# Performance work log

Measured on AMD Instinct MI355X. Metric: run time of the kernel, lower is better.

Reference implementation:

```python
import jax, jax.numpy as jnp
import numpy as np

N_NODES = 50000
N_ENT = 100000
N_REL = 200
DE = 100
DR = 100
B = 16
E2 = 600000
U = 500


def setup_inputs() -> dict:
    key = jax.random.key(0)
    ks = jax.random.split(key, 16)
    f32 = jnp.float32
    return {
        "entity_table": jax.random.normal(ks[0], (N_ENT, DE), f32),
        "relation_table": jax.random.normal(ks[1], (N_REL, DR), f32),
        "total_unseen_embedding": jax.random.normal(ks[2], (U, DE), f32),
        "att_mu": jax.random.normal(ks[3], (2 * N_REL, B), f32) * 0.1,
        "basis_mu": jax.random.normal(ks[4], (B, DE + DR, DE), f32) * 0.05,
        "root_mu": jax.random.normal(ks[5], (DE, DE), f32) * 0.1,
        "bias_mu": jnp.zeros((DE,), f32),
        "att_sigma": jax.random.normal(ks[6], (2 * N_REL, B), f32) * 0.1,
        "basis_sigma": jax.random.normal(ks[7], (B, DE + DR, DE), f32) * 0.05,
        "root_sigma": jax.random.normal(ks[8], (DE, DE), f32) * 0.1,
        "bias_sigma": jnp.zeros((DE,), f32),
        "node_id": jax.random.randint(ks[9], (N_NODES,), 0, N_ENT),
        "edge_index": jax.random.randint(ks[10], (2, E2), 0, N_NODES),
        "edge_type": jax.random.randint(ks[11], (E2,), 0, 2 * N_REL),
        "rel_index": jax.random.randint(ks[12], (E2,), 0, N_REL),
        "unseen_index": jax.random.randint(ks[13], (U,), 0, N_NODES),
    }


def gen_conv(m, edge_type, dst, x, att, basis, root, bias, n_nodes):
    """Basis-decomposed relational conv with mean aggregation (GENConv).

    m: [E, in] per-edge concat(x_src, rel_emb); msg_e = m_e @ (att[type_e] @ basis).
    Computed as sum_b coeff[:, b] * (m @ basis[b]) to avoid an [E, in, out] gather.
    """
    coeff = att[edge_type]  # [E, B]
    msg = coeff[:, 0:1] * (m @ basis[0])
    for b in range(1, basis.shape[0]):
        msg = msg + coeff[:, b:b + 1] * (m @ basis[b])
    agg = jax.ops.segment_sum(msg, dst, num_segments=n_nodes)  # [N, out]
    cnt = jax.ops.segment_sum(jnp.ones((m.shape[0],), m.dtype), dst,
                              num_segments=n_nodes)
    agg = agg / jnp.maximum(cnt, 1.0)[:, None]  # scatter-mean, empty nodes -> 0
    return agg + x @ root + bias


def reference(entity_table, relation_table, total_unseen_embedding,
              att_mu, basis_mu, root_mu, bias_mu,
              att_sigma, basis_sigma, root_sigma, bias_sigma,
              node_id, edge_index, edge_type, rel_index, unseen_index):
    x = entity_table[node_id]  # [N, De]
    x = x.at[unseen_index].set(total_unseen_embedding)
    rel_emb = relation_table[rel_index]  # [E, Dr]
    src, dst = edge_index[0], edge_index[1]
    m = jnp.concatenate([x[src], rel_emb], axis=1)  # [E, De+Dr]
    n = x.shape[0]
    mu = gen_conv(m, edge_type, dst, x, att_mu, basis_mu, root_mu, bias_mu, n)
    logvar = gen_conv(m, edge_type, dst, x, att_sigma, basis_sigma,
                      root_sigma, bias_sigma, n)
    # eval mode: reparameterize -> mu, dropout -> identity
    unseen = mu[unseen_index]
    return unseen, mu[unseen_index], logvar[unseen_index]
```

## Files before the change

### kernel.cpp

```cpp
#include <hip/hip_runtime.h>
#include <stdint.h>

#define E2V     600000
#define NNODES  50000
#define UCNT    500
#define DE      100
#define DOUT    100
#define NB      16
#define KTOT    3328
#define KCH     104
#define MROWS   512
#define HASHN   2048
#define HCAP    64
#define NREG    586
#define ECAP    96
#define TRB     832

using short8 = __attribute__((ext_vector_type(8))) short;
using f32x4  = __attribute__((ext_vector_type(4))) float;

static constexpr size_t align256(size_t x){ return (x + 255) & ~size_t(255); }
static constexpr size_t OFF_HCNT = 0;
static constexpr size_t OFF_IHEA = align256(OFF_HCNT + NREG*4);
static constexpr size_t OFF_INEX = OFF_IHEA + MROWS*4;
static constexpr size_t OFF_HBUF = align256(OFF_INEX + MROWS*4);
static constexpr size_t OFF_GM   = align256(OFF_HBUF + (size_t)NREG*HCAP*4);
static constexpr size_t OFF_GS   = OFF_GM + (size_t)MROWS*KTOT*2;
static constexpr size_t OFF_BTM  = align256(OFF_GS + (size_t)MROWS*KTOT*2);
static constexpr size_t OFF_BTS  = OFF_BTM + (size_t)DOUT*KTOT*2;

__device__ __forceinline__ unsigned short f2b(float f){
    uint32_t u = __float_as_uint(f);
    uint32_t r = (u + 0x7FFFu + ((u >> 16) & 1u)) >> 16;
    return (unsigned short)r;
}

__device__ __forceinline__ uint32_t hh(int key){
    return (((uint32_t)key * 2654435761u) >> 16) & (HASHN - 1);
}
__device__ __forceinline__ void hins(int* hk, int* hv, int key, int val){
    uint32_t idx = hh(key);
    while (true){
        int k = hk[idx];
        if (k == key){ atomicMax(&hv[idx], val); return; }
        if (k == -1){
            int old = atomicCAS(&hk[idx], -1, key);
            if (old == -1 || old == key){ atomicMax(&hv[idx], val); return; }
        }
        idx = (idx + 1) & (HASHN - 1);
    }
}
__device__ __forceinline__ int hlook(const int* hk, const int* hv, int key){
    uint32_t idx = hh(key);
    while (true){
        int k = hk[idx];
        if (k == key) return hv[idx];
        if (k == -1)  return -1;
        idx = (idx + 1) & (HASHN - 1);
    }
}

__device__ __forceinline__ float bt_src(const float* __restrict__ basis,
                                        const float* __restrict__ root,
                                        const float* __restrict__ bias,
                                        int k, int j){
    if (j >= 100) return 0.f;
    if (k < 3200) return basis[k*100 + j];
    if (k < 3300) return root[(k-3200)*100 + j];
    if (k == 3300) return bias[j];
    return 0.f;
}

__global__ __launch_bounds__(256) void k1(
        const int* __restrict__ unseen_index, const int* __restrict__ eidx,
        int* __restrict__ hcnt, uint32_t* __restrict__ hbuf,
        int* __restrict__ ihead, int* __restrict__ inext,
        const float* __restrict__ bm, const float* __restrict__ bs,
        const float* __restrict__ rm, const float* __restrict__ rs,
        const float* __restrict__ qm, const float* __restrict__ qs,
        unsigned short* __restrict__ btm, unsigned short* __restrict__ bts){
    __shared__ int hk[HASHN], hv[HASHN];
    __shared__ float tile[32][33];
    __shared__ uint32_t sHit[HCAP];
    __shared__ int sN, sIH[MROWS];
    int bx = blockIdx.x, tid = threadIdx.x;

    if (bx < NREG){
        for (int i = tid; i < HASHN; i += 256){ hk[i] = -1; hv[i] = -1; }
        if (tid == 0) sN = 0;
        __syncthreads();
        for (int u = tid; u < UCNT; u += 256) hins(hk, hv, unseen_index[u], u);
        __syncthreads();
        int e0 = bx*1024 + tid*4;
        if (e0 < E2V){
            int4 d = *(const int4*)(eidx + E2V + e0);
            int s;
            s = hlook(hk, hv, d.x); if (s >= 0){ int p = atomicAdd(&sN,1); if (p < HCAP) sHit[p] = ((uint32_t)s<<21)|(uint32_t)(e0);   }
            s = hlook(hk, hv, d.y); if (s >= 0){ int p = atomicAdd(&sN,1); if (p < HCAP) sHit[p] = ((uint32_t)s<<21)|(uint32_t)(e0+1); }
            s = hlook(hk, hv, d.z); if (s >= 0){ int p = atomicAdd(&sN,1); if (p < HCAP) sHit[p] = ((uint32_t)s<<21)|(uint32_t)(e0+2); }
            s = hlook(hk, hv, d.w); if (s >= 0){ int p = atomicAdd(&sN,1); if (p < HCAP) sHit[p] = ((uint32_t)s<<21)|(uint32_t)(e0+3); }
        }
        __syncthreads();
        int n = sN < HCAP ? sN : HCAP;
        if (tid == 0) hcnt[bx] = n;
        if (tid < n) hbuf[bx*HCAP + tid] = sHit[tid];
        return;
    }
    if (bx < NREG + TRB){
        int b2 = bx - NREG;
        int kt = b2 % KCH, jt = (b2 / KCH) & 3, br = b2 / (KCH*4);
        const float* basis = br ? bs : bm;
        const float* root  = br ? rs : rm;
        const float* bias  = br ? qs : qm;
        unsigned short* bt = br ? bts : btm;
        int k0 = kt*32, j0 = jt*32;
        int tx = tid & 31, ty = tid >> 5;
        for (int r = ty; r < 32; r += 8)
            tile[r][tx] = bt_src(basis, root, bias, k0 + r, j0 + tx);
        __syncthreads();
        for (int r = ty; r < 32; r += 8){
            int j = j0 + r;
            if (j < 100) bt[(size_t)j*KTOT + k0 + tx] = f2b(tile[tx][r]);
        }
        return;
    }
    for (int i = tid; i < HASHN; i += 256){ hk[i] = -1; hv[i] = -1; }
    for (int i = tid; i < MROWS; i += 256) sIH[i] = -1;
    __syncthreads();
    for (int u = tid; u < UCNT; u += 256) hins(hk, hv, unseen_index[u], u);
    __syncthreads();
    for (int u = tid; u < UCNT; u += 256){
        int slot = hlook(hk, hv, unseen_index[u]);
        inext[u] = atomicExch(&sIH[slot], u);
    }
    __syncthreads();
    for (int i = tid; i < MROWS; i += 256) ihead[i] = sIH[i];
}

__global__ __launch_bounds__(256) void k_g(
        const int* __restrict__ hcnt, const uint32_t* __restrict__ hbuf,
        const int* __restrict__ unseen_index,
        const int* __restrict__ eidx,
        const int* __restrict__ etype, const int* __restrict__ rel_index,
        const int* __restrict__ node_id,
        const float* __restrict__ ent, const float* __restrict__ unseen,
        const float* __restrict__ rel,
        const float* __restrict__ am, const float* __restrict__ as_,
        unsigned short* __restrict__ Gm, unsigned short* __restrict__ Gs){
    int slot = blockIdx.x;
    int tid  = threadIdx.x;
    __shared__ int hk[HASHN], hv[HASHN];
    __shared__ int sEdge[ECAP], sNE;
    __shared__ __align__(16) float sM[8][200];
    __shared__ __align__(16) float sAm[8][16], sAs[8][16];
    __shared__ const float* sPX[8];
    __shared__ const float* sPR[8];
    __shared__ int sT[8];

    for (int i = tid; i < HASHN; i += 256){ hk[i] = -1; hv[i] = -1; }
    if (tid == 0) sNE = 0;
    __syncthreads();
    for (int u = tid; u < UCNT; u += 256) hins(hk, hv, unseen_index[u], u);
    __syncthreads();
    for (int r = tid; r < NREG; r += 256){
        int c = hcnt[r];
        for (int i = 0; i < c; ++i){
            uint32_t h = hbuf[r*HCAP + i];
            if ((int)(h >> 21) == slot){
                int p = atomicAdd(&sNE, 1);
                if (p < ECAP) sEdge[p] = (int)(h & 0x1FFFFFu);
            }
        }
    }
    __syncthreads();
    int nT = sNE;
    int nE = nT > ECAP ? ECAP : nT;

    float gm[16], gs[16];
    #pragma unroll
    for (int b = 0; b < NB; ++b){ gm[b] = 0.f; gs[b] = 0.f; }

    for (int c0 = 0; c0 < nE; c0 += 8){
        int kc = nE - c0; if (kc > 8) kc = 8;
        if (tid < kc){
            int e = sEdge[c0 + tid];
            sT[tid] = etype[e];
            int s = eidx[e];
            int p = hlook(hk, hv, s);
            sPX[tid] = (p >= 0) ? unseen + (size_t)p*DE : ent + (size_t)node_id[s]*DE;
            sPR[tid] = rel + (size_t)rel_index[e]*DE;
        }
        __syncthreads();
        for (int q = tid; q < kc*50; q += 256){
            int eL = q / 50, s = q % 50;
            const float* base = (s < 25) ? sPX[eL] : sPR[eL];
            int off = (s < 25) ? s*4 : (s-25)*4;
            float4 v = *(const float4*)(base + off);
            int kb = (s < 25) ? s*4 : (s-25)*4 + 100;
            *(float4*)&sM[eL][kb] = v;
        }
        if (tid < kc*16){
            int eL = tid >> 4, b = tid & 15;
            int t = sT[eL];
            sAm[eL][b] = am[t*NB + b];
            sAs[eL][b] = as_[t*NB + b];
        }
        __syncthreads();
        if (tid < 200){
            for (int e = 0; e < kc; ++e){
                float mk = sM[e][tid];
                const float4* pa = (const float4*)&sAm[e][0];
                const float4* ps = (const float4*)&sAs[e][0];
                #pragma unroll
                for (int q = 0; q < 4; ++q){
                    float4 va = pa[q], vs = ps[q];
                    gm[q*4+0] += va.x*mk; gm[q*4+1] += va.y*mk;
                    gm[q*4+2] += va.z*mk; gm[q*4+3] += va.w*mk;
                    gs[q*4+0] += vs.x*mk; gs[q*4+1] += vs.y*mk;
                    gs[q*4+2] += vs.z*mk; gs[q*4+3] += vs.w*mk;
                }
            }
        }
        __syncthreads();
    }
    size_t row = (size_t)slot * KTOT;
    float inv = 1.f / fmaxf((float)nT, 1.f);
    if (tid < 200){
        #pragma unroll
        for (int b = 0; b < NB; ++b){
            Gm[row + b*200 + tid] = f2b(gm[b] * inv);
            Gs[row + b*200 + tid] = f2b(gs[b] * inv);
        }
    }
    if (tid < 100){
        float xv = (slot < UCNT) ? unseen[(size_t)slot*DE + tid] : 0.f;
        unsigned short h = f2b(xv);
        Gm[row + 3200 + tid] = h; Gs[row + 3200 + tid] = h;
    } else if (tid == 100){
        Gm[row + 3300] = f2b(1.f); Gs[row + 3300] = f2b(1.f);
    } else if (tid > 100 && tid < 128){
        Gm[row + 3200 + tid] = 0; Gs[row + 3200 + tid] = 0;
    }
}

__global__ __launch_bounds__(512) void k_gemm(
        const unsigned short* __restrict__ Gm, const unsigned short* __restrict__ Gs,
        const unsigned short* __restrict__ Btm, const unsigned short* __restrict__ Bts,
        const int* __restrict__ ihead, const int* __restrict__ inext,
        float* __restrict__ out){
    __shared__ f32x4 red[512];
    int bid = blockIdx.x;
    int br  = bid / 224;
    int w2  = bid % 224;
    int m16 = w2 & 31;
    int jt  = w2 >> 5;
    int wv  = threadIdx.x >> 6;
    int lane = threadIdx.x & 63;
    const unsigned short* A  = br ? Gs : Gm;
    const unsigned short* Bt = br ? Bts : Btm;
    int rowa = lane & 15, ko = (lane >> 4) * 8;
    int j0 = (jt == 6) ? 84 : jt*16;
    int col = j0 + rowa;
    const unsigned short* ap = A  + (size_t)(m16*16 + rowa)*KTOT + ko + wv*416;
    const unsigned short* bp = Bt + (size_t)col*KTOT + ko + wv*416;
    f32x4 acc = {0.f, 0.f, 0.f, 0.f};
    #pragma unroll
    for (int kc = 0; kc < 13; ++kc){
        short8 av = *(const short8*)(ap + kc*32);
        short8 bv = *(const short8*)(bp + kc*32);
        acc = __builtin_amdgcn_mfma_f32_16x16x32_bf16(av, bv, acc, 0, 0, 0);
    }
    red[threadIdx.x] = acc;
    __syncthreads();
    if (threadIdx.x < 64){
        #pragma unroll
        for (int w = 1; w < 8; ++w){
            f32x4 o = red[threadIdx.x + w*64];
            acc[0] += o[0]; acc[1] += o[1]; acc[2] += o[2]; acc[3] += o[3];
        }
        if (jt < 6 || col >= 96){
            int r0 = m16*16 + (lane >> 4)*4;
            #pragma unroll
            for (int r = 0; r < 4; ++r){
                int u = ihead[r0 + r];
                while (u >= 0){
                    if (br == 0){
                        out[(size_t)u*100 + col] = acc[r];
                        out[(size_t)(UCNT + u)*100 + col] = acc[r];
                    } else {
                        out[(size_t)(2*UCNT + u)*100 + col] = acc[r];
                    }
                    u = inext[u];
                }
            }
        }
    }
}

extern "C" void kernel_launch(void* const* d_in, const int* in_sizes, int n_in,
                              void* d_out, int out_size, void* d_ws, size_t ws_size,
                              hipStream_t stream){
    const float* ent        = (const float*)d_in[0];
    const float* rel_table  = (const float*)d_in[1];
    const float* unseen_emb = (const float*)d_in[2];
    const float* att_mu     = (const float*)d_in[3];
    const float* basis_mu   = (const float*)d_in[4];
    const float* root_mu    = (const float*)d_in[5];
    const float* bias_mu    = (const float*)d_in[6];
    const float* att_sig    = (const float*)d_in[7];
    const float* basis_sig  = (const float*)d_in[8];
    const float* root_sig   = (const float*)d_in[9];
    const float* bias_sig   = (const float*)d_in[10];
    const int* node_id      = (const int*)d_in[11];
    const int* edge_index   = (const int*)d_in[12];
    const int* edge_type    = (const int*)d_in[13];
    const int* rel_index    = (const int*)d_in[14];
    const int* unseen_index = (const int*)d_in[15];
    float* out = (float*)d_out;
    char* ws = (char*)d_ws;

    int* hcnt       = (int*)(ws + OFF_HCNT);
    int* ihead      = (int*)(ws + OFF_IHEA);
    int* inext      = (int*)(ws + OFF_INEX);
    uint32_t* hbuf  = (uint32_t*)(ws + OFF_HBUF);
    unsigned short* Gm  = (unsigned short*)(ws + OFF_GM);
    unsigned short* Gs  = (unsigned short*)(ws + OFF_GS);
    unsigned short* Btm = (unsigned short*)(ws + OFF_BTM);
    unsigned short* Bts = (unsigned short*)(ws + OFF_BTS);

    k1<<<NREG + TRB + 1, 256, 0, stream>>>(unseen_index, edge_index,
        hcnt, hbuf, ihead, inext,
        basis_mu, basis_sig, root_mu, root_sig, bias_mu, bias_sig, Btm, Bts);
    k_g<<<MROWS, 256, 0, stream>>>(hcnt, hbuf, unseen_index, edge_index, edge_type,
        rel_index, node_id, ent, unseen_emb, rel_table, att_mu, att_sig, Gm, Gs);
    k_gemm<<<448, 512, 0, stream>>>(Gm, Gs, Btm, Bts, ihead, inext, out);
}
```

Baseline: 49.71 us.

## Resolve source unseen-slot in k1, drop per-block hash rebuild in k_g

The hit records grow to 64 bits so k1 can also look up the edge source in the unseen hash and store that slot. k_g then reads the slot from the record instead of rebuilding a 2048-entry shared hash table of 500 unseen nodes in each of its 512 blocks. This removes the init, insert and lookup work and about 16KB of LDS per block. The GEMM kernel also issues all 13 A/B loads before the MFMA chain to hide memory latency, at the cost of more registers per thread.

Result: no change. 48.74 us (-2.0%).

```diff
diff --git a/kernel.cpp b/kernel.cpp
--- a/kernel.cpp
+++ b/kernel.cpp
@@ -8,7 +8,6 @@
 #define DOUT    100
 #define NB      16
 #define KTOT    3328
-#define KCH     104
 #define MROWS   512
 #define HASHN   2048
 #define HCAP    64
@@ -24,7 +23,7 @@
 static constexpr size_t OFF_IHEA = align256(OFF_HCNT + NREG*4);
 static constexpr size_t OFF_INEX = OFF_IHEA + MROWS*4;
 static constexpr size_t OFF_HBUF = align256(OFF_INEX + MROWS*4);
-static constexpr size_t OFF_GM   = align256(OFF_HBUF + (size_t)NREG*HCAP*4);
+static constexpr size_t OFF_GM   = align256(OFF_HBUF + (size_t)NREG*HCAP*8);
 static constexpr size_t OFF_GS   = OFF_GM + (size_t)MROWS*KTOT*2;
 static constexpr size_t OFF_BTM  = align256(OFF_GS + (size_t)MROWS*KTOT*2);
 static constexpr size_t OFF_BTS  = OFF_BTM + (size_t)DOUT*KTOT*2;
@@ -73,7 +72,7 @@
 
 __global__ __launch_bounds__(256) void k1(
         const int* __restrict__ unseen_index, const int* __restrict__ eidx,
-        int* __restrict__ hcnt, uint32_t* __restrict__ hbuf,
+        int* __restrict__ hcnt, uint64_t* __restrict__ hbuf,
         int* __restrict__ ihead, int* __restrict__ inext,
         const float* __restrict__ bm, const float* __restrict__ bs,
         const float* __restrict__ rm, const float* __restrict__ rs,
@@ -81,7 +80,7 @@
         unsigned short* __restrict__ btm, unsigned short* __restrict__ bts){
     __shared__ int hk[HASHN], hv[HASHN];
     __shared__ float tile[32][33];
-    __shared__ uint32_t sHit[HCAP];
+    __shared__ uint64_t sHit[HCAP];
     __shared__ int sN, sIH[MROWS];
     int bx = blockIdx.x, tid = threadIdx.x;
 
@@ -94,11 +93,19 @@
         int e0 = bx*1024 + tid*4;
         if (e0 < E2V){
             int4 d = *(const int4*)(eidx + E2V + e0);
-            int s;
-            s = hlook(hk, hv, d.x); if (s >= 0){ int p = atomicAdd(&sN,1); if (p < HCAP) sHit[p] = ((uint32_t)s<<21)|(uint32_t)(e0);   }
-            s = hlook(hk, hv, d.y); if (s >= 0){ int p = atomicAdd(&sN,1); if (p < HCAP) sHit[p] = ((uint32_t)s<<21)|(uint32_t)(e0+1); }
-            s = hlook(hk, hv, d.z); if (s >= 0){ int p = atomicAdd(&sN,1); if (p < HCAP) sHit[p] = ((uint32_t)s<<21)|(uint32_t)(e0+2); }
-            s = hlook(hk, hv, d.w); if (s >= 0){ int p = atomicAdd(&sN,1); if (p < HCAP) sHit[p] = ((uint32_t)s<<21)|(uint32_t)(e0+3); }
+            #pragma unroll
+            for (int j = 0; j < 4; ++j){
+                int dn = (j==0) ? d.x : (j==1) ? d.y : (j==2) ? d.z : d.w;
+                int s = hlook(hk, hv, dn);
+                if (s >= 0){
+                    int e = e0 + j;
+                    int srcp = hlook(hk, hv, eidx[e]);
+                    int p = atomicAdd(&sN, 1);
+                    if (p < HCAP)
+                        sHit[p] = ((uint64_t)(uint32_t)(srcp + 1) << 32)
+                                | ((uint64_t)(uint32_t)s << 20) | (uint64_t)(uint32_t)e;
+                }
+            }
         }
         __syncthreads();
         int n = sN < HCAP ? sN : HCAP;
@@ -108,7 +115,7 @@
     }
     if (bx < NREG + TRB){
         int b2 = bx - NREG;
-        int kt = b2 % KCH, jt = (b2 / KCH) & 3, br = b2 / (KCH*4);
+        int kt = b2 % 104, jt = (b2 / 104) & 3, br = b2 / 416;
         const float* basis = br ? bs : bm;
         const float* root  = br ? rs : rm;
         const float* bias  = br ? qs : qm;
@@ -138,8 +145,7 @@
 }
 
 __global__ __launch_bounds__(256) void k_g(
-        const int* __restrict__ hcnt, const uint32_t* __restrict__ hbuf,
-        const int* __restrict__ unseen_index,
+        const int* __restrict__ hcnt, const uint64_t* __restrict__ hbuf,
         const int* __restrict__ eidx,
         const int* __restrict__ etype, const int* __restrict__ rel_index,
         const int* __restrict__ node_id,
@@ -149,26 +155,26 @@
         unsigned short* __restrict__ Gm, unsigned short* __restrict__ Gs){
     int slot = blockIdx.x;
     int tid  = threadIdx.x;
-    __shared__ int hk[HASHN], hv[HASHN];
     __shared__ int sEdge[ECAP], sNE;
+    __shared__ short sSrc[ECAP];
     __shared__ __align__(16) float sM[8][200];
     __shared__ __align__(16) float sAm[8][16], sAs[8][16];
     __shared__ const float* sPX[8];
     __shared__ const float* sPR[8];
     __shared__ int sT[8];
 
-    for (int i = tid; i < HASHN; i += 256){ hk[i] = -1; hv[i] = -1; }
     if (tid == 0) sNE = 0;
-    __syncthreads();
-    for (int u = tid; u < UCNT; u += 256) hins(hk, hv, unseen_index[u], u);
     __syncthreads();
     for (int r = tid; r < NREG; r += 256){
         int c = hcnt[r];
         for (int i = 0; i < c; ++i){
-            uint32_t h = hbuf[r*HCAP + i];
-            if ((int)(h >> 21) == slot){
+            uint64_t h = hbuf[r*HCAP + i];
+            if ((int)((h >> 20) & 0xFFFu) == slot){
                 int p = atomicAdd(&sNE, 1);
-                if (p < ECAP) sEdge[p] = (int)(h & 0x1FFFFFu);
+                if (p < ECAP){
+                    sEdge[p] = (int)(h & 0xFFFFFu);
+                    sSrc[p]  = (short)((int)(uint32_t)(h >> 32) - 1);
+                }
             }
         }
     }
@@ -185,9 +191,9 @@
         if (tid < kc){
             int e = sEdge[c0 + tid];
             sT[tid] = etype[e];
-            int s = eidx[e];
-            int p = hlook(hk, hv, s);
-            sPX[tid] = (p >= 0) ? unseen + (size_t)p*DE : ent + (size_t)node_id[s]*DE;
+            int srcp = sSrc[c0 + tid];
+            sPX[tid] = (srcp >= 0) ? unseen + (size_t)srcp*DE
+                                   : ent + (size_t)node_id[eidx[e]]*DE;
             sPR[tid] = rel + (size_t)rel_index[e]*DE;
         }
         __syncthreads();
@@ -263,13 +269,16 @@
     int col = j0 + rowa;
     const unsigned short* ap = A  + (size_t)(m16*16 + rowa)*KTOT + ko + wv*416;
     const unsigned short* bp = Bt + (size_t)col*KTOT + ko + wv*416;
+    short8 avs[13], bvs[13];
+    #pragma unroll
+    for (int kc = 0; kc < 13; ++kc){
+        avs[kc] = *(const short8*)(ap + kc*32);
+        bvs[kc] = *(const short8*)(bp + kc*32);
+    }
     f32x4 acc = {0.f, 0.f, 0.f, 0.f};
     #pragma unroll
-    for (int kc = 0; kc < 13; ++kc){
-        short8 av = *(const short8*)(ap + kc*32);
-        short8 bv = *(const short8*)(bp + kc*32);
-        acc = __builtin_amdgcn_mfma_f32_16x16x32_bf16(av, bv, acc, 0, 0, 0);
-    }
+    for (int kc = 0; kc < 13; ++kc)
+        acc = __builtin_amdgcn_mfma_f32_16x16x32_bf16(avs[kc], bvs[kc], acc, 0, 0, 0);
     red[threadIdx.x] = acc;
     __syncthreads();
     if (threadIdx.x < 64){
@@ -322,7 +331,7 @@
     int* hcnt       = (int*)(ws + OFF_HCNT);
     int* ihead      = (int*)(ws + OFF_IHEA);
     int* inext      = (int*)(ws + OFF_INEX);
-    uint32_t* hbuf  = (uint32_t*)(ws + OFF_HBUF);
+    uint64_t* hbuf  = (uint64_t*)(ws + OFF_HBUF);
     unsigned short* Gm  = (unsigned short*)(ws + OFF_GM);
     unsigned short* Gs  = (unsigned short*)(ws + OFF_GS);
     unsigned short* Btm = (unsigned short*)(ws + OFF_BTM);
@@ -331,7 +340,7 @@
     k1<<<NREG + TRB + 1, 256, 0, stream>>>(unseen_index, edge_index,
         hcnt, hbuf, ihead, inext,
         basis_mu, basis_sig, root_mu, root_sig, bias_mu, bias_sig, Btm, Bts);
-    k_g<<<MROWS, 256, 0, stream>>>(hcnt, hbuf, unseen_index, edge_index, edge_type,
+    k_g<<<MROWS, 256, 0, stream>>>(hcnt, hbuf, edge_index, edge_type,
         rel_index, node_id, ent, unseen_emb, rel_table, att_mu, att_sig, Gm, Gs);
     k_gemm<<<448, 512, 0, stream>>>(Gm, Gs, Btm, Bts, ihead, inext, out);
 }
```
